# Performance work log

Hardware: AMD Instinct MI355X
Metric: run time of the kernel (lower is better)

Reference implementation:

```python
import jax, jax.numpy as jnp
import numpy as np

B, S, E = 4, 1024, 1280
H = 16
D = E // H  # 80


def rotate_half(x):
    x1, x2 = jnp.split(x, 2, axis=-1)
    return jnp.concatenate([-x2, x1], axis=-1)


def setup_inputs() -> dict:
    key = jax.random.key(0)
    ks = jax.random.split(key, 12)
    sc = 0.02
    x = jax.random.normal(ks[0], (B, S, E), dtype=jnp.float32)
    # variable per-item sequence lengths (each <= S), cumulative
    lens = np.array([1024, 896, 768, 640], dtype=np.int32)
    cu_seqlens = jnp.asarray(np.concatenate([[0], np.cumsum(lens)]), dtype=jnp.int32)
    # rotary cos/sin for positions 0..S-1, head_dim D
    inv_freq = 1.0 / (10000.0 ** (np.arange(0, D, 2, dtype=np.float32) / D))
    t = np.arange(S, dtype=np.float32)
    freqs = np.outer(t, inv_freq)               # [S, D/2]
    emb = np.concatenate([freqs, freqs], axis=-1)  # [S, D]
    cos = jnp.asarray(np.cos(emb), dtype=jnp.float32)
    sin = jnp.asarray(np.sin(emb), dtype=jnp.float32)
    wq = jax.random.normal(ks[1], (E, E), dtype=jnp.float32) * sc
    bq = jax.random.normal(ks[2], (E,), dtype=jnp.float32) * sc
    wk = jax.random.normal(ks[3], (E, E), dtype=jnp.float32) * sc
    bk = jax.random.normal(ks[4], (E,), dtype=jnp.float32) * sc
    wv = jax.random.normal(ks[5], (E, E), dtype=jnp.float32) * sc
    bv = jax.random.normal(ks[6], (E,), dtype=jnp.float32) * sc
    wo = jax.random.normal(ks[7], (E, E), dtype=jnp.float32) * sc
    bo = jax.random.normal(ks[8], (E,), dtype=jnp.float32) * sc
    return {"x": x, "cu_seqlens": cu_seqlens, "cos": cos, "sin": sin,
            "wq": wq, "bq": bq, "wk": wk, "bk": bk, "wv": wv, "bv": bv,
            "wo": wo, "bo": bo}


def reference(x, cu_seqlens, cos, sin, wq, bq, wk, bk, wv, bv, wo, bo):
    b, s, e = x.shape
    h, d = H, D
    # QKV projections (nn.Linear: x @ W^T + b)
    q = (x @ wq.T + bq).reshape(b, s, h, d)
    k = (x @ wk.T + bk).reshape(b, s, h, d)
    v = (x @ wv.T + bv).reshape(b, s, h, d)
    # rotary embedding (apply_rotary_pos_emb, 'normal')
    c = cos[None, :, None, :]  # [1, s, 1, d]
    sn = sin[None, :, None, :]
    q = q * c + rotate_half(q) * sn
    k = k * c + rotate_half(k) * sn
    # patch attention mask from cu_seqlens (flatten_batch=False):
    # token i attends to token j iff i < len_b and j < len_b
    seq_lens = cu_seqlens[1:] - cu_seqlens[:-1]          # [b]
    idx = jnp.arange(s)
    valid = idx[None, :] < seq_lens[:, None]             # [b, s]
    mask = valid[:, None, :, None] & valid[:, None, None, :]  # [b, 1, s, s]
    # SDPA, non-causal
    scale = 1.0 / jnp.sqrt(jnp.asarray(d, dtype=q.dtype))
    scores = jnp.einsum("bqhd,bkhd->bhqk", q, k) * scale
    scores = jnp.where(mask, scores, jnp.asarray(-1e9, dtype=scores.dtype))
    attn = jax.nn.softmax(scores, axis=-1)
    out = jnp.einsum("bhqk,bkhd->bqhd", attn, v)         # [b, s, h, d]
    out = out.reshape(b, s, e)
    # output projection
    return out @ wo.T + bo
```

## Files before the change

kernel.cpp:

```cpp
#include <hip/hip_runtime.h>
#include <hip/hip_bf16.h>

#define B_ 4
#define S_ 1024
#define E_ 1280
#define H_ 16
#define D_ 80
#define M_ (B_*S_)

typedef __hip_bfloat16 bf16;
using bf16x8 = __attribute__((ext_vector_type(8))) short;
using f32x4  = __attribute__((ext_vector_type(4))) float;

__device__ __forceinline__ float b2f(bf16 x){ return __bfloat162float(x); }
__device__ __forceinline__ bf16  f2b(float x){ return __float2bfloat16(x); }
__device__ __forceinline__ void  stf(float* p, float v){ *p = v; }
__device__ __forceinline__ void  stf(bf16*  p, float v){ *p = f2b(v); }

__device__ __forceinline__ void gload_lds16(const void* g, void* l) {
    __builtin_amdgcn_global_load_lds(
        (const __attribute__((address_space(1))) unsigned int*)g,
        (__attribute__((address_space(3))) unsigned int*)l, 16, 0, 0);
}

__global__ __launch_bounds__(256) void cvt_kernel(
    const float* __restrict__ s0, const float* __restrict__ s1,
    const float* __restrict__ s2, const float* __restrict__ s3,
    const float* __restrict__ s4,
    bf16* __restrict__ d0, bf16* __restrict__ d1, bf16* __restrict__ d2,
    bf16* __restrict__ d3, bf16* __restrict__ d4,
    int n0, int n1)
{
    const float* s; bf16* d; int n;
    switch (blockIdx.y) {
        case 0: s = s0; d = d0; n = n0; break;
        case 1: s = s1; d = d1; n = n1; break;
        case 2: s = s2; d = d2; n = n1; break;
        case 3: s = s3; d = d3; n = n1; break;
        default: s = s4; d = d4; n = n1; break;
    }
    int i = (blockIdx.x * 256 + threadIdx.x) * 8;
    if (i >= n) return;
    float4 a = *(const float4*)(s + i);
    float4 b = *(const float4*)(s + i + 4);
    bf16 t[8];
    t[0]=f2b(a.x); t[1]=f2b(a.y); t[2]=f2b(a.z); t[3]=f2b(a.w);
    t[4]=f2b(b.x); t[5]=f2b(b.y); t[6]=f2b(b.z); t[7]=f2b(b.w);
    *(uint4*)(d + i) = *(const uint4*)t;
}

template<typename TC, bool VT_OUT>
__global__ __launch_bounds__(256) void mfma_gemm_bt(
    const bf16* __restrict__ A,
    const bf16* __restrict__ W0, const bf16* __restrict__ W1, const bf16* __restrict__ W2,
    const float* __restrict__ b0, const float* __restrict__ b1, const float* __restrict__ b2,
    TC* __restrict__ C0, TC* __restrict__ C1, TC* __restrict__ C2,
    int K, int N, int ntiles)
{
    const int mat = blockIdx.y / ntiles;
    const int bn  = (blockIdx.y % ntiles) * 128;
    const int bm  = blockIdx.x * 128;
    const bf16* W; const float* bias; TC* C;
    if (mat == 0)      { W = W0; bias = b0; C = C0; }
    else if (mat == 1) { W = W1; bias = b1; C = C1; }
    else               { W = W2; bias = b2; C = C2; }

    __shared__ bf16 As[2][128][32];
    __shared__ bf16 Ws[2][128][32];

    const int tid  = threadIdx.x;
    const int lane = tid & 63;
    const int wv   = tid >> 6;
    const int wm   = (wv & 1) * 64;
    const int wn   = (wv >> 1) * 64;
    const int srow = wv * 16 + (lane >> 2);
    const int scol = (lane & 3) * 8;

    f32x4 acc[4][4] = {};

    for (int k0 = 0; k0 < K; k0 += 64) {
        __syncthreads();
        #pragma unroll
        for (int p = 0; p < 2; p++) {
            const int kc = k0 + p*32 + scol;
            gload_lds16(A + (size_t)(bm + srow)      * K + kc, &As[p][wv*16][0]);
            gload_lds16(A + (size_t)(bm + 64 + srow) * K + kc, &As[p][64 + wv*16][0]);
            gload_lds16(W + (size_t)(bn + srow)      * K + kc, &Ws[p][wv*16][0]);
            gload_lds16(W + (size_t)(bn + 64 + srow) * K + kc, &Ws[p][64 + wv*16][0]);
        }
        __syncthreads();

        const int fr = lane & 15;
        const int kq = (lane >> 4) * 8;
        #pragma unroll
        for (int p = 0; p < 2; p++) {
            bf16x8 af[4], wf[4];
            #pragma unroll
            for (int t = 0; t < 4; t++) {
                af[t] = *(const bf16x8*)&As[p][wm + t*16 + fr][kq];
                wf[t] = *(const bf16x8*)&Ws[p][wn + t*16 + fr][kq];
            }
            #pragma unroll
            for (int mt = 0; mt < 4; mt++)
                #pragma unroll
                for (int nt = 0; nt < 4; nt++)
                    acc[mt][nt] = __builtin_amdgcn_mfma_f32_16x16x32_bf16(
                        af[mt], wf[nt], acc[mt][nt], 0, 0, 0);
        }
    }

    const int col_l = lane & 15;
    const int row_l = (lane >> 4) * 4;

    if (VT_OUT && mat == 2) {
        const int btok = bm >> 10;
        const int keyb = (bm & 1023) + wm + row_l;
        #pragma unroll
        for (int nt = 0; nt < 4; nt++) {
            const int n = bn + wn + nt*16 + col_l;
            const float bv = bias[n];
            const int hh = n / 80, dd = n % 80;
            bf16* vbase = (bf16*)C + ((size_t)(btok*H_ + hh)*D_ + dd)*S_ + keyb;
            #pragma unroll
            for (int mt = 0; mt < 4; mt++) {
                union { bf16 h[4]; uint2 u; } t4;
                #pragma unroll
                for (int r = 0; r < 4; r++) t4.h[r] = f2b(acc[mt][nt][r] + bv);
                *(uint2*)&vbase[mt*16] = t4.u;
            }
        }
    } else {
        #pragma unroll
        for (int nt = 0; nt < 4; nt++) {
            const int n = bn + wn + nt*16 + col_l;
            const float bv = bias[n];
            #pragma unroll
            for (int mt = 0; mt < 4; mt++) {
                #pragma unroll
                for (int r = 0; r < 4; r++) {
                    const int m = bm + wm + mt*16 + row_l + r;
                    stf(&C[(size_t)m * N + n], acc[mt][nt][r] + bv);
                }
            }
        }
    }
}

__device__ __forceinline__ void rope8(const bf16* lo, const bf16* hi,
                                      const float* cp, const float* sp,
                                      float mul, uint4* out_lo, uint4* out_hi)
{
    union { uint4 u; bf16 h[8]; } li, hi_, lo_o, hi_o;
    li.u  = *(const uint4*)lo;
    hi_.u = *(const uint4*)hi;
    #pragma unroll
    for (int u = 0; u < 8; u++) {
        float x1 = b2f(li.h[u]), x2 = b2f(hi_.h[u]);
        float c = cp[u], s = sp[u];
        lo_o.h[u] = f2b((x1*c - x2*s) * mul);
        hi_o.h[u] = f2b((x2*c + x1*s) * mul);
    }
    *out_lo = lo_o.u;
    *out_hi = hi_o.u;
}

__global__ __launch_bounds__(256, 2) void attn_mfma(
    const bf16* __restrict__ q, const bf16* __restrict__ k, const bf16* __restrict__ vt,
    const int* __restrict__ cu, const float* __restrict__ cosp, const float* __restrict__ sinp,
    bf16* __restrict__ o)
{
    __shared__ __align__(16) char smem[51456];
    bf16* Qs  = (bf16*)smem;
    bf16* Ks  = (bf16*)(smem + 26624);
    bf16* VTs = (bf16*)(smem + 39936);

    const int L  = blockIdx.x;
    const int qt = L >> 6;
    const int g  = L & 63;
    const int b  = g >> 4;
    const int h  = g & 15;

    const int tid = threadIdx.x;
    const int lane = tid & 63, wv = tid >> 6;
    const int quad = lane >> 4, l15 = lane & 15;
    const int q0 = qt * 128;
    const int len = cu[b + 1] - cu[b];
    const float scale = 0.11180339887498949f;

    #pragma unroll
    for (int i = 0; i < 3; i++) {
        int c = tid + i * 256;
        if (c < 640) {
            int row = c / 5, pc = c % 5;
            int s = q0 + row;
            const bf16* src = q + (size_t)(b*S_ + s)*E_ + h*D_ + pc*8;
            uint4 olo, ohi;
            rope8(src, src + 40, cosp + s*D_ + pc*8, sinp + s*D_ + pc*8, scale, &olo, &ohi);
            *(uint4*)&Qs[row*104 + pc*8]      = olo;
            *(uint4*)&Qs[row*104 + (pc+5)*8]  = ohi;
        }
    }
    {
        uint4 z = make_uint4(0,0,0,0);
        int row = tid >> 1, c8 = 10 + (tid & 1);
        *(uint4*)&Qs[row*104 + c8*8] = z;
        if (tid < 128) *(uint4*)&Ks[row*104 + c8*8] = z;
    }
    __syncthreads();

    bf16x8 qf[2][3];
    #pragma unroll
    for (int m = 0; m < 2; m++)
        #pragma unroll
        for (int ks = 0; ks < 3; ks++)
            qf[m][ks] = *(const bf16x8*)&Qs[(wv*32 + m*16 + l15)*104 + ks*32 + quad*8];

    float m_r[2][4], l_r[2][4];
    #pragma unroll
    for (int m = 0; m < 2; m++)
        #pragma unroll
        for (int r = 0; r < 4; r++) { m_r[m][r] = -1e30f; l_r[m][r] = 0.f; }
    f32x4 o_acc[2][5] = {};
    bf16* PT = (bf16*)(smem + wv * 4608);

    const bool q_full = (q0 + 128) <= len;

    for (int kt = 0; kt < 16; kt++) {
        __syncthreads();
        #pragma unroll
        for (int i = 0; i < 2; i++) {
            int c = tid + i * 256;
            if (c < 320) {
                int row = c / 5, pc = c % 5;
                int s = kt*64 + row;
                const bf16* src = k + (size_t)(b*S_ + s)*E_ + h*D_ + pc*8;
                uint4 olo, ohi;
                rope8(src, src + 40, cosp + s*D_ + pc*8, sinp + s*D_ + pc*8, 1.0f, &olo, &ohi);
                *(uint4*)&Ks[row*104 + pc*8]      = olo;
                *(uint4*)&Ks[row*104 + (pc+5)*8]  = ohi;
            }
        }
        #pragma unroll
        for (int i = 0; i < 3; i++) {
            int c = tid + i * 256;
            if (c < 640) {
                int d = c >> 3, kc = c & 7;
                *(uint4*)&VTs[d*72 + kc*8] =
                    *(const uint4*)(vt + ((size_t)(b*H_ + h)*D_ + d)*S_ + kt*64 + kc*8);
            }
        }
        __syncthreads();

        f32x4 s4[2][4];
        #pragma unroll
        for (int nt = 0; nt < 4; nt++) {
            f32x4 a0 = {}, a1 = {};
            #pragma unroll
            for (int ks = 0; ks < 3; ks++) {
                bf16x8 kf = *(const bf16x8*)&Ks[(nt*16 + l15)*104 + ks*32 + quad*8];
                a0 = __builtin_amdgcn_mfma_f32_16x16x32_bf16(qf[0][ks], kf, a0, 0, 0, 0);
                a1 = __builtin_amdgcn_mfma_f32_16x16x32_bf16(qf[1][ks], kf, a1, 0, 0, 0);
            }
            s4[0][nt] = a0; s4[1][nt] = a1;
        }

        const bool full = q_full && (kt*64 + 64) <= len;
        bool vk[4];
        #pragma unroll
        for (int nt = 0; nt < 4; nt++) vk[nt] = (kt*64 + nt*16 + l15) < len;

        #pragma unroll
        for (int m = 0; m < 2; m++) {
            float sv[4][4];
            if (full) {
                #pragma unroll
                for (int r = 0; r < 4; r++)
                    #pragma unroll
                    for (int nt = 0; nt < 4; nt++)
                        sv[nt][r] = s4[m][nt][r];
            } else {
                #pragma unroll
                for (int r = 0; r < 4; r++) {
                    const bool vq = (q0 + wv*32 + m*16 + quad*4 + r) < len;
                    #pragma unroll
                    for (int nt = 0; nt < 4; nt++)
                        sv[nt][r] = (vq && vk[nt]) ? s4[m][nt][r] : -1e9f;
                }
            }
            float rmax[4];
            #pragma unroll
            for (int r = 0; r < 4; r++)
                rmax[r] = fmaxf(fmaxf(sv[0][r], sv[1][r]), fmaxf(sv[2][r], sv[3][r]));
            #pragma unroll
            for (int st = 1; st < 16; st <<= 1)
                #pragma unroll
                for (int r = 0; r < 4; r++)
                    rmax[r] = fmaxf(rmax[r], __shfl_xor(rmax[r], st, 64));
            float mnew[4], alpha[4], rsum[4], p[4][4];
            #pragma unroll
            for (int r = 0; r < 4; r++) {
                mnew[r]  = fmaxf(m_r[m][r], rmax[r]);
                alpha[r] = __expf(m_r[m][r] - mnew[r]);
                float a = 0.f;
                #pragma unroll
                for (int nt = 0; nt < 4; nt++) { p[nt][r] = __expf(sv[nt][r] - mnew[r]); a += p[nt][r]; }
                rsum[r] = a;
            }
            #pragma unroll
            for (int st = 1; st < 16; st <<= 1)
                #pragma unroll
                for (int r = 0; r < 4; r++)
                    rsum[r] += __shfl_xor(rsum[r], st, 64);
            #pragma unroll
            for (int r = 0; r < 4; r++) {
                l_r[m][r] = l_r[m][r] * alpha[r] + rsum[r];
                m_r[m][r] = mnew[r];
            }
            #pragma unroll
            for (int dt = 0; dt < 5; dt++)
                #pragma unroll
                for (int r = 0; r < 4; r++)
                    o_acc[m][dt][r] *= alpha[r];
            #pragma unroll
            for (int nt = 0; nt < 4; nt++)
                #pragma unroll
                for (int r = 0; r < 4; r++)
                    PT[(m*16 + quad*4 + r)*72 + nt*16 + l15] = f2b(p[nt][r]);
        }

        bf16x8 pa[2][2];
        #pragma unroll
        for (int m = 0; m < 2; m++)
            #pragma unroll
            for (int ks = 0; ks < 2; ks++)
                pa[m][ks] = *(const bf16x8*)&PT[(m*16 + l15)*72 + ks*32 + quad*8];
        #pragma unroll
        for (int dt = 0; dt < 5; dt++) {
            #pragma unroll
            for (int ks = 0; ks < 2; ks++) {
                bf16x8 vf = *(const bf16x8*)&VTs[(dt*16 + l15)*72 + ks*32 + quad*8];
                o_acc[0][dt] = __builtin_amdgcn_mfma_f32_16x16x32_bf16(pa[0][ks], vf, o_acc[0][dt], 0, 0, 0);
                o_acc[1][dt] = __builtin_amdgcn_mfma_f32_16x16x32_bf16(pa[1][ks], vf, o_acc[1][dt], 0, 0, 0);
            }
        }
    }

    #pragma unroll
    for (int m = 0; m < 2; m++)
        #pragma unroll
        for (int r = 0; r < 4; r++) {
            const float inv = 1.0f / l_r[m][r];
            size_t row_g = (size_t)(b*S_ + q0 + wv*32 + m*16 + quad*4 + r);
            #pragma unroll
            for (int dt = 0; dt < 5; dt++)
                o[row_g*E_ + h*D_ + dt*16 + l15] = f2b(o_acc[m][dt][r] * inv);
        }
}

extern "C" void kernel_launch(void* const* d_in, const int* in_sizes, int n_in,
                              void* d_out, int out_size, void* d_ws, size_t ws_size,
                              hipStream_t stream)
{
    const float* x    = (const float*)d_in[0];
    const int*   cu   = (const int*)  d_in[1];
    const float* cosp = (const float*)d_in[2];
    const float* sinp = (const float*)d_in[3];
    const float* wq   = (const float*)d_in[4];
    const float* bq   = (const float*)d_in[5];
    const float* wk   = (const float*)d_in[6];
    const float* bk   = (const float*)d_in[7];
    const float* wv   = (const float*)d_in[8];
    const float* bv   = (const float*)d_in[9];
    const float* wo   = (const float*)d_in[10];
    const float* bo   = (const float*)d_in[11];
    float* out = (float*)d_out;

    bf16* q   = (bf16*)d_ws;
    bf16* kk  = q   + (size_t)M_ * E_;
    bf16* vt  = kk  + (size_t)M_ * E_;
    bf16* ao  = vt  + (size_t)M_ * E_;
    bf16* xb  = ao  + (size_t)M_ * E_;
    bf16* wqb = xb  + (size_t)M_ * E_;
    bf16* wkb = wqb + (size_t)E_ * E_;
    bf16* wvb = wkb + (size_t)E_ * E_;
    bf16* wob = wvb + (size_t)E_ * E_;

    cvt_kernel<<<dim3(2560, 5), 256, 0, stream>>>(
        x, wq, wk, wv, wo, xb, wqb, wkb, wvb, wob, M_*E_, E_*E_);

    mfma_gemm_bt<bf16, true><<<dim3(M_/128, 30), 256, 0, stream>>>(
        xb, wqb, wkb, wvb, bq, bk, bv, q, kk, vt, E_, E_, 10);

    attn_mfma<<<512, 256, 0, stream>>>(q, kk, vt, cu, cosp, sinp, ao);

    mfma_gemm_bt<float, false><<<dim3(M_/128, 10), 256, 0, stream>>>(
        ao, wob, wob, wob, bo, bo, bo, out, out, out, E_, E_, 10);
}
```

Baseline: 281.9 us.

## Halve attention query tile to 64 rows and double grid size

Shrinks each attention block from 128 to 64 query rows, with one 16-row MFMA tile per wave, and launches 1024 blocks instead of 512. Shared memory and register use drop, and launch bounds allow 4 blocks per CU, to raise occupancy and fill more CUs. The trade-off is that each K/V tile, including the recomputed RoPE on K, is loaded and processed twice as often across the grid.

Result: faster. 274.3 us (-2.7%).

```diff
diff --git a/kernel.cpp b/kernel.cpp
--- a/kernel.cpp
+++ b/kernel.cpp
@@ -164,15 +164,15 @@
     *out_hi = hi_o.u;
 }
 
-__global__ __launch_bounds__(256, 2) void attn_mfma(
+__global__ __launch_bounds__(256, 4) void attn_mfma(
     const bf16* __restrict__ q, const bf16* __restrict__ k, const bf16* __restrict__ vt,
     const int* __restrict__ cu, const float* __restrict__ cosp, const float* __restrict__ sinp,
     bf16* __restrict__ o)
 {
-    __shared__ __align__(16) char smem[51456];
+    __shared__ __align__(16) char smem[38144];
     bf16* Qs  = (bf16*)smem;
-    bf16* Ks  = (bf16*)(smem + 26624);
-    bf16* VTs = (bf16*)(smem + 39936);
+    bf16* Ks  = (bf16*)(smem + 13312);
+    bf16* VTs = (bf16*)(smem + 26624);
 
     const int L  = blockIdx.x;
     const int qt = L >> 6;
@@ -183,14 +183,14 @@
     const int tid = threadIdx.x;
     const int lane = tid & 63, wv = tid >> 6;
     const int quad = lane >> 4, l15 = lane & 15;
-    const int q0 = qt * 128;
+    const int q0 = qt * 64;
     const int len = cu[b + 1] - cu[b];
     const float scale = 0.11180339887498949f;
 
     #pragma unroll
-    for (int i = 0; i < 3; i++) {
+    for (int i = 0; i < 2; i++) {
         int c = tid + i * 256;
-        if (c < 640) {
+        if (c < 320) {
             int row = c / 5, pc = c % 5;
             int s = q0 + row;
             const bf16* src = q + (size_t)(b*S_ + s)*E_ + h*D_ + pc*8;
@@ -200,30 +200,26 @@
             *(uint4*)&Qs[row*104 + (pc+5)*8]  = ohi;
         }
     }
-    {
+    if (tid < 128) {
         uint4 z = make_uint4(0,0,0,0);
         int row = tid >> 1, c8 = 10 + (tid & 1);
         *(uint4*)&Qs[row*104 + c8*8] = z;
-        if (tid < 128) *(uint4*)&Ks[row*104 + c8*8] = z;
+        *(uint4*)&Ks[row*104 + c8*8] = z;
     }
     __syncthreads();
 
-    bf16x8 qf[2][3];
-    #pragma unroll
-    for (int m = 0; m < 2; m++)
-        #pragma unroll
-        for (int ks = 0; ks < 3; ks++)
-            qf[m][ks] = *(const bf16x8*)&Qs[(wv*32 + m*16 + l15)*104 + ks*32 + quad*8];
-
-    float m_r[2][4], l_r[2][4];
-    #pragma unroll
-    for (int m = 0; m < 2; m++)
-        #pragma unroll
-        for (int r = 0; r < 4; r++) { m_r[m][r] = -1e30f; l_r[m][r] = 0.f; }
-    f32x4 o_acc[2][5] = {};
-    bf16* PT = (bf16*)(smem + wv * 4608);
-
-    const bool q_full = (q0 + 128) <= len;
+    bf16x8 qf[3];
+    #pragma unroll
+    for (int ks = 0; ks < 3; ks++)
+        qf[ks] = *(const bf16x8*)&Qs[(wv*16 + l15)*104 + ks*32 + quad*8];
+
+    float m_r[4], l_r[4];
+    #pragma unroll
+    for (int r = 0; r < 4; r++) { m_r[r] = -1e30f; l_r[r] = 0.f; }
+    f32x4 o_acc[5] = {};
+    bf16* PT = (bf16*)(smem + wv * 2304);
+
+    const bool q_full = (q0 + 64) <= len;
 
     for (int kt = 0; kt < 16; kt++) {
         __syncthreads();
@@ -251,110 +247,101 @@
         }
         __syncthreads();
 
-        f32x4 s4[2][4];
+        f32x4 s4[4];
         #pragma unroll
         for (int nt = 0; nt < 4; nt++) {
-            f32x4 a0 = {}, a1 = {};
+            f32x4 a0 = {};
             #pragma unroll
             for (int ks = 0; ks < 3; ks++) {
                 bf16x8 kf = *(const bf16x8*)&Ks[(nt*16 + l15)*104 + ks*32 + quad*8];
-                a0 = __builtin_amdgcn_mfma_f32_16x16x32_bf16(qf[0][ks], kf, a0, 0, 0, 0);
-                a1 = __builtin_amdgcn_mfma_f32_16x16x32_bf16(qf[1][ks], kf, a1, 0, 0, 0);
-            }
-            s4[0][nt] = a0; s4[1][nt] = a1;
+                a0 = __builtin_amdgcn_mfma_f32_16x16x32_bf16(qf[ks], kf, a0, 0, 0, 0);
+            }
+            s4[nt] = a0;
         }
 
         const bool full = q_full && (kt*64 + 64) <= len;
-        bool vk[4];
-        #pragma unroll
-        for (int nt = 0; nt < 4; nt++) vk[nt] = (kt*64 + nt*16 + l15) < len;
-
-        #pragma unroll
-        for (int m = 0; m < 2; m++) {
-            float sv[4][4];
-            if (full) {
-                #pragma unroll
-                for (int r = 0; r < 4; r++)
-                    #pragma unroll
-                    for (int nt = 0; nt < 4; nt++)
-                        sv[nt][r] = s4[m][nt][r];
-            } else {
-                #pragma unroll
-                for (int r = 0; r < 4; r++) {
-                    const bool vq = (q0 + wv*32 + m*16 + quad*4 + r) < len;
-                    #pragma unroll
-                    for (int nt = 0; nt < 4; nt++)
-                        sv[nt][r] = (vq && vk[nt]) ? s4[m][nt][r] : -1e9f;
-                }
-            }
-            float rmax[4];
-            #pragma unroll
-            for (int r = 0; r < 4; r++)
-                rmax[r] = fmaxf(fmaxf(sv[0][r], sv[1][r]), fmaxf(sv[2][r], sv[3][r]));
-            #pragma unroll
-            for (int st = 1; st < 16; st <<= 1)
-                #pragma unroll
-                for (int r = 0; r < 4; r++)
-                    rmax[r] = fmaxf(rmax[r], __shfl_xor(rmax[r], st, 64));
-            float mnew[4], alpha[4], rsum[4], p[4][4];
+
+        float sv[4][4];
+        if (full) {
+            #pragma unroll
+            for (int r = 0; r < 4; r++)
+                #pragma unroll
+                for (int nt = 0; nt < 4; nt++)
+                    sv[nt][r] = s4[nt][r];
+        } else {
+            bool vk[4];
+            #pragma unroll
+            for (int nt = 0; nt < 4; nt++) vk[nt] = (kt*64 + nt*16 + l15) < len;
             #pragma unroll
             for (int r = 0; r < 4; r++) {
-                mnew[r]  = fmaxf(m_r[m][r], rmax[r]);
-                alpha[r] = __expf(m_r[m][r] - mnew[r]);
-                float a = 0.f;
-                #pragma unroll
-                for (int nt = 0; nt < 4; nt++) { p[nt][r] = __expf(sv[nt][r] - mnew[r]); a += p[nt][r]; }
-                rsum[r] = a;
-            }
-            #pragma unroll
-            for (int st = 1; st < 16; st <<= 1)
-                #pragma unroll
-                for (int r = 0; r < 4; r++)
-                    rsum[r] += __shfl_xor(rsum[r], st, 64);
-            #pragma unroll
-            for (int r = 0; r < 4; r++) {
-                l_r[m][r] = l_r[m][r] * alpha[r] + rsum[r];
-                m_r[m][r] = mnew[r];
-            }
-            #pragma unroll
-            for (int dt = 0; dt < 5; dt++)
-                #pragma unroll
-                for (int r = 0; r < 4; r++)
-                    o_acc[m][dt][r] *= alpha[r];
-            #pragma unroll
-            for (int nt = 0; nt < 4; nt++)
-                #pragma unroll
-                for (int r = 0; r < 4; r++)
-                    PT[(m*16 + quad*4 + r)*72 + nt*16 + l15] = f2b(p[nt][r]);
-        }
-
-        bf16x8 pa[2][2];
-        #pragma unroll
-        for (int m = 0; m < 2; m++)
-            #pragma unroll
-            for (int ks = 0; ks < 2; ks++)
-                pa[m][ks] = *(const bf16x8*)&PT[(m*16 + l15)*72 + ks*32 + quad*8];
+                const bool vq = (q0 + wv*16 + quad*4 + r) < len;
+                #pragma unroll
+                for (int nt = 0; nt < 4; nt++)
+                    sv[nt][r] = (vq && vk[nt]) ? s4[nt][r] : -1e9f;
+            }
+        }
+        float rmax[4];
+        #pragma unroll
+        for (int r = 0; r < 4; r++)
+            rmax[r] = fmaxf(fmaxf(sv[0][r], sv[1][r]), fmaxf(sv[2][r], sv[3][r]));
+        #pragma unroll
+        for (int st = 1; st < 16; st <<= 1)
+            #pragma unroll
+            for (int r = 0; r < 4; r++)
+                rmax[r] = fmaxf(rmax[r], __shfl_xor(rmax[r], st, 64));
+        float mnew[4], alpha[4], rsum[4], p[4][4];
+        #pragma unroll
+        for (int r = 0; r < 4; r++) {
+            mnew[r]  = fmaxf(m_r[r], rmax[r]);
+            alpha[r] = __expf(m_r[r] - mnew[r]);
+            float a = 0.f;
+            #pragma unroll
+            for (int nt = 0; nt < 4; nt++) { p[nt][r] = __expf(sv[nt][r] - mnew[r]); a += p[nt][r]; }
+            rsum[r] = a;
+        }
+        #pragma unroll
+        for (int st = 1; st < 16; st <<= 1)
+            #pragma unroll
+            for (int r = 0; r < 4; r++)
+                rsum[r] += __shfl_xor(rsum[r], st, 64);
+        #pragma unroll
+        for (int r = 0; r < 4; r++) {
+            l_r[r] = l_r[r] * alpha[r] + rsum[r];
+            m_r[r] = mnew[r];
+        }
+        #pragma unroll
+        for (int dt = 0; dt < 5; dt++)
+            #pragma unroll
+            for (int r = 0; r < 4; r++)
+                o_acc[dt][r] *= alpha[r];
+        #pragma unroll
+        for (int nt = 0; nt < 4; nt++)
+            #pragma unroll
+            for (int r = 0; r < 4; r++)
+                PT[(quad*4 + r)*72 + nt*16 + l15] = f2b(p[nt][r]);
+
+        bf16x8 pa[2];
+        #pragma unroll
+        for (int ks = 0; ks < 2; ks++)
+            pa[ks] = *(const bf16x8*)&PT[l15*72 + ks*32 + quad*8];
         #pragma unroll
         for (int dt = 0; dt < 5; dt++) {
             #pragma unroll
             for (int ks = 0; ks < 2; ks++) {
                 bf16x8 vf = *(const bf16x8*)&VTs[(dt*16 + l15)*72 + ks*32 + quad*8];
-                o_acc[0][dt] = __builtin_amdgcn_mfma_f32_16x16x32_bf16(pa[0][ks], vf, o_acc[0][dt], 0, 0, 0);
-                o_acc[1][dt] = __builtin_amdgcn_mfma_f32_16x16x32_bf16(pa[1][ks], vf, o_acc[1][dt], 0, 0, 0);
-            }
-        }
-    }
-
-    #pragma unroll
-    for (int m = 0; m < 2; m++)
-        #pragma unroll
-        for (int r = 0; r < 4; r++) {
-            const float inv = 1.0f / l_r[m][r];
-            size_t row_g = (size_t)(b*S_ + q0 + wv*32 + m*16 + quad*4 + r);
-            #pragma unroll
-            for (int dt = 0; dt < 5; dt++)
-                o[row_g*E_ + h*D_ + dt*16 + l15] = f2b(o_acc[m][dt][r] * inv);
-        }
+                o_acc[dt] = __builtin_amdgcn_mfma_f32_16x16x32_bf16(pa[ks], vf, o_acc[dt], 0, 0, 0);
+            }
+        }
+    }
+
+    #pragma unroll
+    for (int r = 0; r < 4; r++) {
+        const float inv = 1.0f / l_r[r];
+        size_t row_g = (size_t)(b*S_ + q0 + wv*16 + quad*4 + r);
+        #pragma unroll
+        for (int dt = 0; dt < 5; dt++)
+            o[row_g*E_ + h*D_ + dt*16 + l15] = f2b(o_acc[dt][r] * inv);
+    }
 }
 
 extern "C" void kernel_launch(void* const* d_in, const int* in_sizes, int n_in,
@@ -391,7 +378,7 @@
     mfma_gemm_bt<bf16, true><<<dim3(M_/128, 30), 256, 0, stream>>>(
         xb, wqb, wkb, wvb, bq, bk, bv, q, kk, vt, E_, E_, 10);
 
-    attn_mfma<<<512, 256, 0, stream>>>(q, kk, vt, cu, cosp, sinp, ao);
+    attn_mfma<<<1024, 256, 0, stream>>>(q, kk, vt, cu, cosp, sinp, ao);
 
     mfma_gemm_bt<float, false><<<dim3(M_/128, 10), 256, 0, stream>>>(
         ao, wob, wob, wob, bo, bo, bo, out, out, out, E_, E_, 10);
```
